# Performance work log

Hardware: AMD Instinct MI355X
Metric: run time of the kernel (lower is better)

The kernel has to match this reference:

```python
import jax, jax.numpy as jnp
import numpy as np
from jax import lax

DN = ('NCHW', 'OIHW', 'NCHW')

def conv(x, w, b, stride, pad):
    y = lax.conv_general_dilated(x, w, (stride, stride), [(pad, pad), (pad, pad)], dimension_numbers=DN)
    return y + b[None, :, None, None]

def setup_inputs() -> dict:
    key = jax.random.key(0)
    ks = jax.random.split(key, 16)
    s = 0.05
    inp = {
        'condition': jax.random.normal(ks[0], (16, 1, 256, 256), jnp.float32),
        'w1': jax.random.normal(ks[1], (64, 1, 4, 4), jnp.float32) * s,
        'b1': jnp.zeros((64,), jnp.float32),
        'w2': jax.random.normal(ks[2], (128, 64, 4, 4), jnp.float32) * s,
        'b2': jnp.zeros((128,), jnp.float32),
        'w3': jax.random.normal(ks[3], (128, 128, 3, 3), jnp.float32) * s,
        'b3': jnp.zeros((128,), jnp.float32),
        'r1w1': jax.random.normal(ks[4], (32, 128, 3, 3), jnp.float32) * s,
        'r1b1': jnp.zeros((32,), jnp.float32),
        'r1w2': jax.random.normal(ks[5], (128, 32, 1, 1), jnp.float32) * s,
        'r1b2': jnp.zeros((128,), jnp.float32),
        'r2w1': jax.random.normal(ks[6], (32, 128, 3, 3), jnp.float32) * s,
        'r2b1': jnp.zeros((32,), jnp.float32),
        'r2w2': jax.random.normal(ks[7], (128, 32, 1, 1), jnp.float32) * s,
        'r2b2': jnp.zeros((128,), jnp.float32),
        'wpre': jax.random.normal(ks[8], (4, 128, 1, 1), jnp.float32) * s,
        'bpre': jnp.zeros((4,), jnp.float32),
        'codebook': jax.random.normal(ks[9], (2048, 4), jnp.float32),
    }
    return inp

def reference(condition, w1, b1, w2, b2, w3, b3, r1w1, r1b1, r1w2, r1b2,
              r2w1, r2b1, r2w2, r2b2, wpre, bpre, codebook):
    # --- conv encoder (VQ-VAE standard) ---
    h = jax.nn.relu(conv(condition, w1, b1, 2, 1))   # [B,64,128,128]
    h = jax.nn.relu(conv(h, w2, b2, 2, 1))           # [B,128,64,64]
    h = conv(h, w3, b3, 1, 1)                        # [B,128,64,64]
    # residual stack: 2 blocks of relu->3x3->relu->1x1, residual add
    for wa, ba, wb, bb in ((r1w1, r1b1, r1w2, r1b2), (r2w1, r2b1, r2w2, r2b2)):
        t = conv(jax.nn.relu(h), wa, ba, 1, 1)
        t = conv(jax.nn.relu(t), wb, bb, 1, 0)
        h = h + t
    h = jax.nn.relu(h)
    z = conv(h, wpre, bpre, 1, 0)                    # [B,4,64,64]
    # --- cosine-distance vector quantization ---
    B, D, H, W = z.shape
    zf = jnp.transpose(z, (0, 2, 3, 1)).reshape(-1, D)          # [BHW, D]
    zn = zf / (jnp.linalg.norm(zf, axis=-1, keepdims=True) + 1e-12)
    en = codebook / (jnp.linalg.norm(codebook, axis=-1, keepdims=True) + 1e-12)
    sim = jnp.einsum('nd,kd->nk', zn, en)                       # cosine similarity
    idx = jnp.argmax(sim, axis=-1)                              # nearest code
    q = codebook[idx].reshape(B, H, W, D)
    c = jnp.transpose(q, (0, 3, 1, 2))                          # [B,4,64,64]
    return c
```

## Files before the change

kernel.cpp:

```cpp
#include <hip/hip_runtime.h>
#include <math.h>


typedef short v8s __attribute__((ext_vector_type(8)));
typedef float v4f __attribute__((ext_vector_type(4)));

#define B_OFF 4194304
#define A_OFF 12582912
#define W2_S 0
#define W3_S 393216
#define WR1_S 835584
#define WR2_S 946176
#define WP1_S 1056768
#define WP2_S 1069056

__device__ inline void limb3(float v, unsigned short& h, unsigned short& m,
                             unsigned short& l) {
    unsigned ub = __float_as_uint(v);
    unsigned hb = ub & 0xffff0000u;
    float r1 = v - __uint_as_float(hb);
    unsigned mb = __float_as_uint(r1) & 0xffff0000u;
    float r2 = r1 - __uint_as_float(mb);
    unsigned lb = __float_as_uint(r2) & 0xffff0000u;
    h = (unsigned short)(hb >> 16);
    m = (unsigned short)(mb >> 16);
    l = (unsigned short)(lb >> 16);
}

struct CfgConv2 {
    static constexpr int NC = 8, NT = 4, OC = 128, ICG = 64, IN_H = 128, IN_W = 128;
    static constexpr bool RELU_IN = false, RELU_OUT = true;
    __device__ static void tap(int c, int t, int& ry, int& rx) {
        int py = (c >> 2) & 1, px = (c >> 1) & 1;
        ry = (t >> 1) - py; rx = (t & 1) - px;
    }
    __device__ static void inaddr(int c, int oy, int r, int X,
                                  int& Yg, int& Xg, int& ic0) {
        int py = (c >> 2) & 1, px = (c >> 1) & 1;
        Yg = 2 * (oy + r - 1) + py; Xg = 2 * X + px; ic0 = (c & 1) * 32;
    }
    __device__ static int widx(int c, int t, int oc, int ic) {
        int py = (c >> 2) & 1, px = (c >> 1) & 1, half = c & 1;
        int dy = 2 * (t >> 1) + (1 - py), dx = 2 * (t & 1) + (1 - px);
        return ((oc * 64 + half * 32 + ic) * 4 + dy) * 4 + dx;
    }
};
struct CfgConv3 {
    static constexpr int NC = 4, NT = 9, OC = 128, ICG = 128, IN_H = 64, IN_W = 64;
    static constexpr bool RELU_IN = false, RELU_OUT = false;
    __device__ static void tap(int c, int t, int& ry, int& rx) {
        ry = t / 3 - 1; rx = t % 3 - 1;
    }
    __device__ static void inaddr(int c, int oy, int r, int X,
                                  int& Yg, int& Xg, int& ic0) {
        Yg = oy + r - 1; Xg = X; ic0 = c * 32;
    }
    __device__ static int widx(int c, int t, int oc, int ic) {
        return ((oc * 128 + c * 32 + ic) * 3 + t / 3) * 3 + t % 3;
    }
};
struct CfgRes {
    static constexpr int NC = 4, NT = 9, OC = 32, ICG = 128, IN_H = 64, IN_W = 64;
    __device__ static int widx(int c, int t, int oc, int ic) {
        return ((oc * 128 + c * 32 + ic) * 3 + t / 3) * 3 + t % 3;
    }
};
struct Cfg1x1 {
    static constexpr int NC = 1, NT = 1, OC = 128;
    __device__ static int widx(int c, int t, int oc, int ic) {
        return oc * 32 + ic;
    }
};

template <typename C>
__device__ inline void repack_one(const float* __restrict__ w,
                                  short* __restrict__ dst, int idx) {
    int s  = idx & 31;
    int oc = (idx >> 5) % C::OC;
    int ct = idx / (32 * C::OC);
    int c = ct / C::NT, t = ct % C::NT;
    float val = w[C::widx(c, t, oc, s)];
    unsigned short h, m, l;
    limb3(val, h, m, l);
    constexpr int NTILE = C::OC / 16;
    int nt = oc >> 4, o = oc & 15, q = s >> 3, j = s & 7;
    int fr = ((q * 16 + o) << 3) + j;
    dst[(((ct * 3 + 0) * NTILE + nt) << 9) + fr] = (short)h;
    dst[(((ct * 3 + 1) * NTILE + nt) << 9) + fr] = (short)m;
    dst[(((ct * 3 + 2) * NTILE + nt) << 9) + fr] = (short)l;
}

__global__ __launch_bounds__(256) void repack_all_k(
    const float* __restrict__ w2, const float* __restrict__ w3,
    const float* __restrict__ r1, const float* __restrict__ r2,
    const float* __restrict__ p1, const float* __restrict__ p2,
    short* __restrict__ base)
{
    int idx = blockIdx.x * 256 + threadIdx.x;
    if (idx < 131072) { repack_one<CfgConv2>(w2, base + W2_S, idx); return; }
    idx -= 131072;
    if (idx < 147456) { repack_one<CfgConv3>(w3, base + W3_S, idx); return; }
    idx -= 147456;
    if (idx < 36864)  { repack_one<CfgRes>(r1, base + WR1_S, idx); return; }
    idx -= 36864;
    if (idx < 36864)  { repack_one<CfgRes>(r2, base + WR2_S, idx); return; }
    idx -= 36864;
    if (idx < 4096)   { repack_one<Cfg1x1>(p1, base + WP1_S, idx); return; }
    idx -= 4096;
    if (idx < 4096)   { repack_one<Cfg1x1>(p2, base + WP2_S, idx); }
}

template <typename C>
__global__ __launch_bounds__(256, 3) void mfma_conv(
    const float* __restrict__ in, const short* __restrict__ repw,
    const float* __restrict__ bias, float* __restrict__ out, int n0)
{
    constexpr int APLANE = 3 * 66 * 32;
    constexpr int NTILE  = C::OC / 16;
    __shared__ __align__(16) short lA[3 * APLANE];

    int tid = threadIdx.x;
    int lane = tid & 63, wv = tid >> 6;
    int n_img = blockIdx.x >> 6, oy = blockIdx.x & 63;

    for (int idx = tid; idx < 3 * 3 * 2 * 16; idx += 256) {
        int plane = idx / 96;
        int rem = idx % 96;
        int rr = rem / 32;
        int hc = (rem / 16) & 1;
        int d = idx & 15;
        ((unsigned*)lA)[plane * 3168 + (rr * 66 + hc * 65) * 16 + d] = 0;
    }

    v4f acc[4][2] = {};
    int nbase = wv * 2;
    int Xq = tid & 15, icp = tid >> 4, quad = lane >> 4;

    float pv[24];
    auto issue_loads = [&](int c) {
#pragma unroll
        for (int it = 0; it < 12; it++) {
            int r = it >> 2, xg = it & 3;
            int X = xg * 16 + Xq;
            int Yg, Xg, ic0;
            C::inaddr(c, oy, r, X, Yg, Xg, ic0);
            float v0 = 0.f, v1 = 0.f;
            if (Yg >= 0 && Yg < C::IN_H) {
                int g = ((n_img * C::ICG + ic0 + 2 * icp) * C::IN_H + Yg) * C::IN_W + Xg;
                v0 = in[g];
                v1 = in[g + C::IN_H * C::IN_W];
            }
            pv[2 * it] = v0; pv[2 * it + 1] = v1;
        }
    };
    auto load_bf = [&](int c, int t, v8s (&dst)[2][3]) {
#pragma unroll
        for (int nt = 0; nt < 2; nt++)
#pragma unroll
            for (int L = 0; L < 3; L++)
                dst[nt][L] = *(const v8s*)(repw +
                    ((((c * C::NT + t) * 3 + L) * NTILE + (nbase + nt)) << 9) +
                    (lane << 3));
    };

    issue_loads(0);

    for (int c = 0; c < C::NC; c++) {
        __syncthreads();
#pragma unroll
        for (int it = 0; it < 12; it++) {
            int r = it >> 2, xg = it & 3;
            int X = xg * 16 + Xq;
            float v0 = pv[2 * it], v1 = pv[2 * it + 1];
            if constexpr (C::RELU_IN) { v0 = fmaxf(v0, 0.f); v1 = fmaxf(v1, 0.f); }
            unsigned short h0, m0, l0, h1, m1, l1;
            limb3(v0, h0, m0, l0);
            limb3(v1, h1, m1, l1);
            int cell = r * 66 + X + 1;
            int f = (cell + (cell >> 2)) & 3;
            int phys = (icp & 3) + 4 * (((icp >> 2) + f) & 3);
            unsigned* pa = (unsigned*)lA + cell * 16 + phys;
            pa[0]        = (unsigned)h0 | ((unsigned)h1 << 16);
            pa[3168]     = (unsigned)m0 | ((unsigned)m1 << 16);
            pa[2 * 3168] = (unsigned)l0 | ((unsigned)l1 << 16);
        }
        __syncthreads();
        if (c + 1 < C::NC) issue_loads(c + 1);

        v8s bf[2][2][3];
        load_bf(c, 0, bf[0]);
#pragma unroll
        for (int t = 0; t < C::NT; t++) {
            constexpr int NTT = C::NT;
            if (t + 1 < NTT) load_bf(c, t + 1, bf[(t + 1) & 1]);
            int ry, rx;
            C::tap(c, t, ry, rx);
#pragma unroll
            for (int mt = 0; mt < 4; mt++) {
                int x = mt * 16 + (lane & 15);
                int cell = (ry + 1) * 66 + (x + rx + 1);
                int f = (cell + (cell >> 2)) & 3;
                int aa = cell * 32 + (((quad + f) & 3) << 3);
                v8s ah = *(const v8s*)&lA[aa];
                v8s am = *(const v8s*)&lA[APLANE + aa];
                v8s al = *(const v8s*)&lA[2 * APLANE + aa];
#pragma unroll
                for (int nt = 0; nt < 2; nt++) {
                    v4f a0 = acc[mt][nt];
                    a0 = __builtin_amdgcn_mfma_f32_16x16x32_bf16(ah, bf[t & 1][nt][0], a0, 0, 0, 0);
                    a0 = __builtin_amdgcn_mfma_f32_16x16x32_bf16(ah, bf[t & 1][nt][1], a0, 0, 0, 0);
                    a0 = __builtin_amdgcn_mfma_f32_16x16x32_bf16(am, bf[t & 1][nt][0], a0, 0, 0, 0);
                    a0 = __builtin_amdgcn_mfma_f32_16x16x32_bf16(am, bf[t & 1][nt][1], a0, 0, 0, 0);
                    a0 = __builtin_amdgcn_mfma_f32_16x16x32_bf16(ah, bf[t & 1][nt][2], a0, 0, 0, 0);
                    a0 = __builtin_amdgcn_mfma_f32_16x16x32_bf16(al, bf[t & 1][nt][0], a0, 0, 0, 0);
                    acc[mt][nt] = a0;
                }
            }
        }
    }
#pragma unroll
    for (int mt = 0; mt < 4; mt++) {
        int x0 = mt * 16 + quad * 4;
#pragma unroll
        for (int nt = 0; nt < 2; nt++) {
            int oc = (nbase + nt) * 16 + (lane & 15);
            float bv = bias[oc];
            float v0 = acc[mt][nt][0] + bv;
            float v1 = acc[mt][nt][1] + bv;
            float v2 = acc[mt][nt][2] + bv;
            float v3 = acc[mt][nt][3] + bv;
            if constexpr (C::RELU_OUT) {
                v0 = fmaxf(v0, 0.f); v1 = fmaxf(v1, 0.f);
                v2 = fmaxf(v2, 0.f); v3 = fmaxf(v3, 0.f);
            }
            float4 o = make_float4(v0, v1, v2, v3);
            *(float4*)&out[(((n0 + n_img) * C::OC + oc) * 64 + oy) * 64 + x0] = o;
        }
    }
}

__global__ __launch_bounds__(256, 4) void mfma_res(
    const float* __restrict__ in, const short* __restrict__ repw,
    const float* __restrict__ b1, const short* __restrict__ repp,
    const float* __restrict__ b2, float* __restrict__ out)
{
    constexpr int APLANE = 3 * 66 * 32;
    __shared__ __align__(16) short lA[3 * APLANE];

    int tid = threadIdx.x;
    int lane = tid & 63, wv = tid >> 6;
    int n_img = blockIdx.x >> 6, oy = blockIdx.x & 63;

    for (int idx = tid; idx < 3 * 3 * 2 * 16; idx += 256) {
        int plane = idx / 96;
        int rem = idx % 96;
        int rr = rem / 32;
        int hc = (rem / 16) & 1;
        int d = idx & 15;
        ((unsigned*)lA)[plane * 3168 + (rr * 66 + hc * 65) * 16 + d] = 0;
    }

    v4f acc[2] = {};
    int Xq = tid & 15, icp = tid >> 4, quad = lane >> 4;

    float pv[24];
    auto issue_loads = [&](int c) {
#pragma unroll
        for (int it = 0; it < 12; it++) {
            int r = it >> 2, xg = it & 3;
            int X = xg * 16 + Xq;
            int Yg = oy + r - 1;
            float v0 = 0.f, v1 = 0.f;
            if (Yg >= 0 && Yg < 64) {
                int g = ((n_img * 128 + c * 32 + 2 * icp) * 64 + Yg) * 64 + X;
                v0 = in[g];
                v1 = in[g + 4096];
            }
            pv[2 * it] = v0; pv[2 * it + 1] = v1;
        }
    };

    issue_loads(0);

    for (int c = 0; c < 4; c++) {
        __syncthreads();
#pragma unroll
        for (int it = 0; it < 12; it++) {
            int r = it >> 2, xg = it & 3;
            int X = xg * 16 + Xq;
            float v0 = fmaxf(pv[2 * it], 0.f);
            float v1 = fmaxf(pv[2 * it + 1], 0.f);
            unsigned short h0, m0, l0, h1, m1, l1;
            limb3(v0, h0, m0, l0);
            limb3(v1, h1, m1, l1);
            int cell = r * 66 + X + 1;
            int f = (cell + (cell >> 2)) & 3;
            int phys = (icp & 3) + 4 * (((icp >> 2) + f) & 3);
            unsigned* pa = (unsigned*)lA + cell * 16 + phys;
            pa[0]        = (unsigned)h0 | ((unsigned)h1 << 16);
            pa[3168]     = (unsigned)m0 | ((unsigned)m1 << 16);
            pa[2 * 3168] = (unsigned)l0 | ((unsigned)l1 << 16);
        }
        __syncthreads();
        if (c + 1 < 4) issue_loads(c + 1);

        v8s bf[2][2][3];
        auto load_bf = [&](int t, v8s (&dst)[2][3]) {
#pragma unroll
            for (int nt = 0; nt < 2; nt++)
#pragma unroll
                for (int L = 0; L < 3; L++)
                    dst[nt][L] = *(const v8s*)(repw +
                        ((((c * 9 + t) * 3 + L) * 2 + nt) << 9) + (lane << 3));
        };
        load_bf(0, bf[0]);
#pragma unroll
        for (int t = 0; t < 9; t++) {
            if (t + 1 < 9) load_bf(t + 1, bf[(t + 1) & 1]);
            int ry = t / 3 - 1, rx = t % 3 - 1;
            int x = wv * 16 + (lane & 15);
            int cell = (ry + 1) * 66 + (x + rx + 1);
            int f = (cell + (cell >> 2)) & 3;
            int aa = cell * 32 + (((quad + f) & 3) << 3);
            v8s ah = *(const v8s*)&lA[aa];
            v8s am = *(const v8s*)&lA[APLANE + aa];
            v8s al = *(const v8s*)&lA[2 * APLANE + aa];
#pragma unroll
            for (int nt = 0; nt < 2; nt++) {
                v4f a0 = acc[nt];
                a0 = __builtin_amdgcn_mfma_f32_16x16x32_bf16(ah, bf[t & 1][nt][0], a0, 0, 0, 0);
                a0 = __builtin_amdgcn_mfma_f32_16x16x32_bf16(ah, bf[t & 1][nt][1], a0, 0, 0, 0);
                a0 = __builtin_amdgcn_mfma_f32_16x16x32_bf16(am, bf[t & 1][nt][0], a0, 0, 0, 0);
                a0 = __builtin_amdgcn_mfma_f32_16x16x32_bf16(am, bf[t & 1][nt][1], a0, 0, 0, 0);
                a0 = __builtin_amdgcn_mfma_f32_16x16x32_bf16(ah, bf[t & 1][nt][2], a0, 0, 0, 0);
                a0 = __builtin_amdgcn_mfma_f32_16x16x32_bf16(al, bf[t & 1][nt][0], a0, 0, 0, 0);
                acc[nt] = a0;
            }
        }
    }

    __syncthreads();
#pragma unroll
    for (int nt = 0; nt < 2; nt++) {
        int ic = nt * 16 + (lane & 15);
        int icp2 = ic >> 1, hilo = ic & 1;
        float bv = b1[ic];
#pragma unroll
        for (int r = 0; r < 4; r++) {
            int x = wv * 16 + quad * 4 + r;
            float v = fmaxf(acc[nt][r] + bv, 0.f);
            unsigned short h, m, l;
            limb3(v, h, m, l);
            int f = (x + (x >> 2)) & 3;
            int phys = (icp2 & 3) + 4 * (((icp2 >> 2) + f) & 3);
            int sa = x * 32 + phys * 2 + hilo;
            lA[sa] = (short)h;
            lA[2048 + sa] = (short)m;
            lA[4096 + sa] = (short)l;
        }
    }
    __syncthreads();

    v4f a2[8] = {};
    {
        int x = wv * 16 + (lane & 15);
        int f = (x + (x >> 2)) & 3;
        int aa = x * 32 + (((quad + f) & 3) << 3);
        v8s ah = *(const v8s*)&lA[aa];
        v8s am = *(const v8s*)&lA[2048 + aa];
        v8s al = *(const v8s*)&lA[4096 + aa];
#pragma unroll
        for (int nt = 0; nt < 8; nt++) {
            v8s bh = *(const v8s*)(repp + ((0 * 8 + nt) << 9) + (lane << 3));
            v8s bm = *(const v8s*)(repp + ((1 * 8 + nt) << 9) + (lane << 3));
            v8s bl = *(const v8s*)(repp + ((2 * 8 + nt) << 9) + (lane << 3));
            v4f a0 = a2[nt];
            a0 = __builtin_amdgcn_mfma_f32_16x16x32_bf16(ah, bh, a0, 0, 0, 0);
            a0 = __builtin_amdgcn_mfma_f32_16x16x32_bf16(ah, bm, a0, 0, 0, 0);
            a0 = __builtin_amdgcn_mfma_f32_16x16x32_bf16(am, bh, a0, 0, 0, 0);
            a0 = __builtin_amdgcn_mfma_f32_16x16x32_bf16(am, bm, a0, 0, 0, 0);
            a0 = __builtin_amdgcn_mfma_f32_16x16x32_bf16(ah, bl, a0, 0, 0, 0);
            a0 = __builtin_amdgcn_mfma_f32_16x16x32_bf16(al, bh, a0, 0, 0, 0);
            a2[nt] = a0;
        }
    }
#pragma unroll
    for (int nt = 0; nt < 8; nt++) {
        int oc = nt * 16 + (lane & 15);
        int x0 = wv * 16 + quad * 4;
        int off = ((n_img * 128 + oc) * 64 + oy) * 64 + x0;
        float4 hv = *(const float4*)&in[off];
        float bv = b2[oc];
        float4 o = make_float4(hv.x + a2[nt][0] + bv, hv.y + a2[nt][1] + bv,
                               hv.z + a2[nt][2] + bv, hv.w + a2[nt][3] + bv);
        *(float4*)&out[off] = o;
    }
}

__global__ __launch_bounds__(256) void conv1_k(
    const float* __restrict__ x, const float* __restrict__ w,
    const float* __restrict__ b, float* __restrict__ out)
{
    int tid = blockIdx.x * 256 + threadIdx.x;
    int n   = tid >> 14;
    int rem = tid & 16383;
    int oy  = rem >> 7;
    int ox  = rem & 127;
    int iy0 = oy * 2 - 1, ix0 = ox * 2 - 1;
    const float* xb = x + n * 65536;
    float v[16];
#pragma unroll
    for (int ky = 0; ky < 4; ky++) {
#pragma unroll
        for (int kx = 0; kx < 4; kx++) {
            int iy = iy0 + ky, ix = ix0 + kx;
            bool ok = (iy >= 0) & (iy < 256) & (ix >= 0) & (ix < 256);
            v[ky * 4 + kx] = ok ? xb[iy * 256 + ix] : 0.f;
        }
    }
    int obase = (n * 64) * 16384 + (oy << 7) + ox;
    for (int oc = 0; oc < 64; oc++) {
        float acc = b[oc];
        const float* wp = w + oc * 16;
#pragma unroll
        for (int k = 0; k < 16; k++) acc = fmaf(v[k], wp[k], acc);
        out[obase + oc * 16384] = fmaxf(acc, 0.f);
    }
}

__global__ __launch_bounds__(256) void prevq_k(
    const float* __restrict__ h, const float* __restrict__ wpre,
    const float* __restrict__ bpre, const float* __restrict__ cb,
    float* __restrict__ out)
{
    __shared__ float4 en[2048];
    for (int i = threadIdx.x; i < 2048; i += 256) {
        float c0 = cb[i * 4 + 0], c1 = cb[i * 4 + 1];
        float c2 = cb[i * 4 + 2], c3 = cb[i * 4 + 3];
        float nrm = sqrtf(c0 * c0 + c1 * c1 + c2 * c2 + c3 * c3) + 1e-12f;
        en[i] = make_float4(c0 / nrm, c1 / nrm, c2 / nrm, c3 / nrm);
    }
    __syncthreads();

    int tid = blockIdx.x * 256 + threadIdx.x;
    int n   = tid >> 12;
    int pos = tid & 4095;
    const float* hb = h + n * 128 * 4096 + pos;
    float z0 = bpre[0], z1 = bpre[1], z2 = bpre[2], z3 = bpre[3];
    for (int ic = 0; ic < 128; ic++) {
        float v = fmaxf(hb[ic * 4096], 0.f);
        z0 = fmaf(v, wpre[ic],       z0);
        z1 = fmaf(v, wpre[128 + ic], z1);
        z2 = fmaf(v, wpre[256 + ic], z2);
        z3 = fmaf(v, wpre[384 + ic], z3);
    }
    float best = -1e30f;
    int   bidx = 0;
    for (int k = 0; k < 2048; k++) {
        float4 e = en[k];
        float s = z0 * e.x + z1 * e.y + z2 * e.z + z3 * e.w;
        if (s > best) { best = s; bidx = k; }
    }
    const float* q = cb + bidx * 4;
    out[(n * 4 + 0) * 4096 + pos] = q[0];
    out[(n * 4 + 1) * 4096 + pos] = q[1];
    out[(n * 4 + 2) * 4096 + pos] = q[2];
    out[(n * 4 + 3) * 4096 + pos] = q[3];
}

extern "C" void kernel_launch(void* const* d_in, const int* in_sizes, int n_in,
                              void* d_out, int out_size, void* d_ws, size_t ws_size,
                              hipStream_t stream)
{
    const float* x    = (const float*)d_in[0];
    const float* w1   = (const float*)d_in[1];
    const float* b1   = (const float*)d_in[2];
    const float* w2   = (const float*)d_in[3];
    const float* b2   = (const float*)d_in[4];
    const float* w3   = (const float*)d_in[5];
    const float* b3   = (const float*)d_in[6];
    const float* r1w1 = (const float*)d_in[7];
    const float* r1b1 = (const float*)d_in[8];
    const float* r1w2 = (const float*)d_in[9];
    const float* r1b2 = (const float*)d_in[10];
    const float* r2w1 = (const float*)d_in[11];
    const float* r2b1 = (const float*)d_in[12];
    const float* r2w2 = (const float*)d_in[13];
    const float* r2b2 = (const float*)d_in[14];
    const float* wpre = (const float*)d_in[15];
    const float* bpre = (const float*)d_in[16];
    const float* cb   = (const float*)d_in[17];
    float* out = (float*)d_out;

    float* ws   = (float*)d_ws;
    short* wsS  = (short*)d_ws;
    float* B = ws + B_OFF;
    float* A = ws + A_OFF;

    repack_all_k<<<1408, 256, 0, stream>>>(w2, w3, r1w1, r2w1, r1w2, r2w2, wsS);

    conv1_k<<<512, 256, 0, stream>>>(x,               w1, b1, A);
    mfma_conv<CfgConv2><<<512, 256, 0, stream>>>(A, wsS + W2_S, b2, B, 0);
    conv1_k<<<512, 256, 0, stream>>>(x + 8 * 65536,   w1, b1, A);
    mfma_conv<CfgConv2><<<512, 256, 0, stream>>>(A, wsS + W2_S, b2, B, 8);

    mfma_conv<CfgConv3><<<1024, 256, 0, stream>>>(B, wsS + W3_S, b3, A, 0);

    mfma_res<<<1024, 256, 0, stream>>>(A, wsS + WR1_S, r1b1, wsS + WP1_S, r1b2, B);
    mfma_res<<<1024, 256, 0, stream>>>(B, wsS + WR2_S, r2b1, wsS + WP2_S, r2b2, A);

    prevq_k<<<256, 256, 0, stream>>>(A, wpre, bpre, cb, out);
}
```

Measured before the change: 485.0 us.

## Double-buffer LDS input tiles and interleave staging with MFMA taps

The conv kernel now keeps two LDS buffers and two register prefetch sets. It stages the next chunk's bf16 limbs into the alternate buffer in slices interleaved between the MFMA tap iterations, and prefetches two chunks ahead, so one barrier per chunk replaces two. The goal is to hide the global-load and conversion latency behind matrix math. In exchange LDS use doubles, register pressure rises, and launch bounds drop from 3 to 2 blocks per CU, which lowers occupancy.

```diff
diff --git a/kernel.cpp b/kernel.cpp
--- a/kernel.cpp
+++ b/kernel.cpp
@@ -111,33 +111,26 @@
 }
 
 template <typename C>
-__global__ __launch_bounds__(256, 3) void mfma_conv(
+__global__ __launch_bounds__(256, 2) void mfma_conv(
     const float* __restrict__ in, const short* __restrict__ repw,
     const float* __restrict__ bias, float* __restrict__ out, int n0)
 {
     constexpr int APLANE = 3 * 66 * 32;
+    constexpr int BUFS   = 3 * APLANE;
     constexpr int NTILE  = C::OC / 16;
-    __shared__ __align__(16) short lA[3 * APLANE];
+    __shared__ __align__(16) short lA[2 * BUFS];
 
     int tid = threadIdx.x;
     int lane = tid & 63, wv = tid >> 6;
     int n_img = blockIdx.x >> 6, oy = blockIdx.x & 63;
 
-    for (int idx = tid; idx < 3 * 3 * 2 * 16; idx += 256) {
-        int plane = idx / 96;
-        int rem = idx % 96;
-        int rr = rem / 32;
-        int hc = (rem / 16) & 1;
-        int d = idx & 15;
-        ((unsigned*)lA)[plane * 3168 + (rr * 66 + hc * 65) * 16 + d] = 0;
-    }
-
-    v4f acc[4][2] = {};
     int nbase = wv * 2;
     int Xq = tid & 15, icp = tid >> 4, quad = lane >> 4;
 
-    float pv[24];
-    auto issue_loads = [&](int c) {
+    v4f acc[4][2] = {};
+    float pvA[24], pvB[24];
+
+    auto issue_loads = [&](int c, float* pv) {
 #pragma unroll
         for (int it = 0; it < 12; it++) {
             int r = it >> 2, xg = it & 3;
@@ -153,6 +146,22 @@
             pv[2 * it] = v0; pv[2 * it + 1] = v1;
         }
     };
+    auto stage_it = [&](int it, short* dst, const float* pv) {
+        int r = it >> 2, xg = it & 3;
+        int X = xg * 16 + Xq;
+        float v0 = pv[2 * it], v1 = pv[2 * it + 1];
+        if constexpr (C::RELU_IN) { v0 = fmaxf(v0, 0.f); v1 = fmaxf(v1, 0.f); }
+        unsigned short h0, m0, l0, h1, m1, l1;
+        limb3(v0, h0, m0, l0);
+        limb3(v1, h1, m1, l1);
+        int cell = r * 66 + X + 1;
+        int f = (cell + (cell >> 2)) & 3;
+        int phys = (icp & 3) + 4 * (((icp >> 2) + f) & 3);
+        unsigned* pa = (unsigned*)dst + cell * 16 + phys;
+        pa[0]        = (unsigned)h0 | ((unsigned)h1 << 16);
+        pa[3168]     = (unsigned)m0 | ((unsigned)m1 << 16);
+        pa[2 * 3168] = (unsigned)l0 | ((unsigned)l1 << 16);
+    };
     auto load_bf = [&](int c, int t, v8s (&dst)[2][3]) {
 #pragma unroll
         for (int nt = 0; nt < 2; nt++)
@@ -163,30 +172,10 @@
                     (lane << 3));
     };
 
-    issue_loads(0);
-
-    for (int c = 0; c < C::NC; c++) {
-        __syncthreads();
-#pragma unroll
-        for (int it = 0; it < 12; it++) {
-            int r = it >> 2, xg = it & 3;
-            int X = xg * 16 + Xq;
-            float v0 = pv[2 * it], v1 = pv[2 * it + 1];
-            if constexpr (C::RELU_IN) { v0 = fmaxf(v0, 0.f); v1 = fmaxf(v1, 0.f); }
-            unsigned short h0, m0, l0, h1, m1, l1;
-            limb3(v0, h0, m0, l0);
-            limb3(v1, h1, m1, l1);
-            int cell = r * 66 + X + 1;
-            int f = (cell + (cell >> 2)) & 3;
-            int phys = (icp & 3) + 4 * (((icp >> 2) + f) & 3);
-            unsigned* pa = (unsigned*)lA + cell * 16 + phys;
-            pa[0]        = (unsigned)h0 | ((unsigned)h1 << 16);
-            pa[3168]     = (unsigned)m0 | ((unsigned)m1 << 16);
-            pa[2 * 3168] = (unsigned)l0 | ((unsigned)l1 << 16);
-        }
-        __syncthreads();
-        if (c + 1 < C::NC) issue_loads(c + 1);
-
+    auto run_chunk = [&](int c, const short* cur, short* nxt,
+                         const float* pvr, float* pvw) {
+        if (c + 2 < C::NC) issue_loads(c + 2, pvw);
+        const bool do_stage = (c + 1 < C::NC);
         v8s bf[2][2][3];
         load_bf(c, 0, bf[0]);
 #pragma unroll
@@ -201,9 +190,9 @@
                 int cell = (ry + 1) * 66 + (x + rx + 1);
                 int f = (cell + (cell >> 2)) & 3;
                 int aa = cell * 32 + (((quad + f) & 3) << 3);
-                v8s ah = *(const v8s*)&lA[aa];
-                v8s am = *(const v8s*)&lA[APLANE + aa];
-                v8s al = *(const v8s*)&lA[2 * APLANE + aa];
+                v8s ah = *(const v8s*)&cur[aa];
+                v8s am = *(const v8s*)&cur[APLANE + aa];
+                v8s al = *(const v8s*)&cur[2 * APLANE + aa];
 #pragma unroll
                 for (int nt = 0; nt < 2; nt++) {
                     v4f a0 = acc[mt][nt];
@@ -216,8 +205,38 @@
                     acc[mt][nt] = a0;
                 }
             }
-        }
-    }
+            if (do_stage) {
+#pragma unroll
+                for (int it = (t * 12) / NTT; it < ((t + 1) * 12) / NTT; it++)
+                    stage_it(it, nxt, pvr);
+            }
+        }
+    };
+
+    issue_loads(0, pvA);
+    issue_loads(1, pvB);
+    for (int idx = tid; idx < 2 * 3 * 3 * 2 * 16; idx += 256) {
+        int buf = idx / 288;
+        int rem = idx % 288;
+        int plane = rem / 96;
+        int rem2 = rem % 96;
+        int rr = rem2 / 32;
+        int hc = (rem2 / 16) & 1;
+        int d = idx & 15;
+        ((unsigned*)lA)[buf * (BUFS / 2) + plane * 3168 + (rr * 66 + hc * 65) * 16 + d] = 0;
+    }
+#pragma unroll
+    for (int it = 0; it < 12; it++) stage_it(it, lA, pvA);
+    __syncthreads();
+
+    for (int c = 0; c < C::NC; c++) {
+        const short* cur = lA + (c & 1) * BUFS;
+        short* nxt = lA + ((c & 1) ^ 1) * BUFS;
+        if ((c & 1) == 0) run_chunk(c, cur, nxt, pvB, pvA);
+        else              run_chunk(c, cur, nxt, pvA, pvB);
+        if (c + 1 < C::NC) __syncthreads();
+    }
+
 #pragma unroll
     for (int mt = 0; mt < 4; mt++) {
         int x0 = mt * 16 + quad * 4;
```

After: 552.8 us. +14.0%, slower.

## Remap mfma_conv waves to 2x2 M/N tiling and split weight prefetch

Applied to the files above, without the earlier changes.

Changes the warp tiling in the MFMA conv kernel: each of 4 waves now computes 2 M-tiles by 4 N-tiles instead of 4 M-tiles by 2 N-tiles. Per tap this halves the LDS A-fragment reads per wave and doubles the global weight fragment loads. Weight loading is split into two halves interleaved with the MFMA groups, which replaces the full double buffer and keeps register pressure down. The risk is more global/L2 traffic for weights, traded against less LDS bandwidth use.

```diff
diff --git a/kernel.cpp b/kernel.cpp
--- a/kernel.cpp
+++ b/kernel.cpp
@@ -117,6 +117,7 @@
 {
     constexpr int APLANE = 3 * 66 * 32;
     constexpr int NTILE  = C::OC / 16;
+    constexpr int NTT    = C::NT;
     __shared__ __align__(16) short lA[3 * APLANE];
 
     int tid = threadIdx.x;
@@ -132,8 +133,9 @@
         ((unsigned*)lA)[plane * 3168 + (rr * 66 + hc * 65) * 16 + d] = 0;
     }
 
-    v4f acc[4][2] = {};
-    int nbase = wv * 2;
+    int mr = wv >> 1, nc = wv & 1;
+    int nbase = nc * 4;
+    v4f acc[2][4] = {};
     int Xq = tid & 15, icp = tid >> 4, quad = lane >> 4;
 
     float pv[24];
@@ -153,13 +155,13 @@
             pv[2 * it] = v0; pv[2 * it + 1] = v1;
         }
     };
-    auto load_bf = [&](int c, int t, v8s (&dst)[2][3]) {
-#pragma unroll
-        for (int nt = 0; nt < 2; nt++)
+    auto load_half = [&](int c, int t, int hp, v8s (&dst)[2][3]) {
+#pragma unroll
+        for (int j = 0; j < 2; j++)
 #pragma unroll
             for (int L = 0; L < 3; L++)
-                dst[nt][L] = *(const v8s*)(repw +
-                    ((((c * C::NT + t) * 3 + L) * NTILE + (nbase + nt)) << 9) +
+                dst[j][L] = *(const v8s*)(repw +
+                    ((((c * NTT + t) * 3 + L) * NTILE + (nbase + hp * 2 + j)) << 9) +
                     (lane << 3));
     };
 
@@ -187,48 +189,64 @@
         __syncthreads();
         if (c + 1 < C::NC) issue_loads(c + 1);
 
-        v8s bf[2][2][3];
-        load_bf(c, 0, bf[0]);
-#pragma unroll
-        for (int t = 0; t < C::NT; t++) {
-            constexpr int NTT = C::NT;
-            if (t + 1 < NTT) load_bf(c, t + 1, bf[(t + 1) & 1]);
+        v8s bf0[2][3], bf1[2][3];
+        load_half(c, 0, 0, bf0);
+#pragma unroll
+        for (int t = 0; t < NTT; t++) {
             int ry, rx;
             C::tap(c, t, ry, rx);
-#pragma unroll
-            for (int mt = 0; mt < 4; mt++) {
-                int x = mt * 16 + (lane & 15);
+            v8s ah[2], am[2], al[2];
+#pragma unroll
+            for (int mti = 0; mti < 2; mti++) {
+                int x = (mr * 2 + mti) * 16 + (lane & 15);
                 int cell = (ry + 1) * 66 + (x + rx + 1);
                 int f = (cell + (cell >> 2)) & 3;
                 int aa = cell * 32 + (((quad + f) & 3) << 3);
-                v8s ah = *(const v8s*)&lA[aa];
-                v8s am = *(const v8s*)&lA[APLANE + aa];
-                v8s al = *(const v8s*)&lA[2 * APLANE + aa];
-#pragma unroll
-                for (int nt = 0; nt < 2; nt++) {
-                    v4f a0 = acc[mt][nt];
-                    a0 = __builtin_amdgcn_mfma_f32_16x16x32_bf16(ah, bf[t & 1][nt][0], a0, 0, 0, 0);
-                    a0 = __builtin_amdgcn_mfma_f32_16x16x32_bf16(ah, bf[t & 1][nt][1], a0, 0, 0, 0);
-                    a0 = __builtin_amdgcn_mfma_f32_16x16x32_bf16(am, bf[t & 1][nt][0], a0, 0, 0, 0);
-                    a0 = __builtin_amdgcn_mfma_f32_16x16x32_bf16(am, bf[t & 1][nt][1], a0, 0, 0, 0);
-                    a0 = __builtin_amdgcn_mfma_f32_16x16x32_bf16(ah, bf[t & 1][nt][2], a0, 0, 0, 0);
-                    a0 = __builtin_amdgcn_mfma_f32_16x16x32_bf16(al, bf[t & 1][nt][0], a0, 0, 0, 0);
-                    acc[mt][nt] = a0;
+                ah[mti] = *(const v8s*)&lA[aa];
+                am[mti] = *(const v8s*)&lA[APLANE + aa];
+                al[mti] = *(const v8s*)&lA[2 * APLANE + aa];
+            }
+            load_half(c, t, 1, bf1);
+#pragma unroll
+            for (int mti = 0; mti < 2; mti++)
+#pragma unroll
+                for (int j = 0; j < 2; j++) {
+                    v4f a0 = acc[mti][j];
+                    a0 = __builtin_amdgcn_mfma_f32_16x16x32_bf16(ah[mti], bf0[j][0], a0, 0, 0, 0);
+                    a0 = __builtin_amdgcn_mfma_f32_16x16x32_bf16(ah[mti], bf0[j][1], a0, 0, 0, 0);
+                    a0 = __builtin_amdgcn_mfma_f32_16x16x32_bf16(am[mti], bf0[j][0], a0, 0, 0, 0);
+                    a0 = __builtin_amdgcn_mfma_f32_16x16x32_bf16(am[mti], bf0[j][1], a0, 0, 0, 0);
+                    a0 = __builtin_amdgcn_mfma_f32_16x16x32_bf16(ah[mti], bf0[j][2], a0, 0, 0, 0);
+                    a0 = __builtin_amdgcn_mfma_f32_16x16x32_bf16(al[mti], bf0[j][0], a0, 0, 0, 0);
+                    acc[mti][j] = a0;
                 }
-            }
-        }
-    }
-#pragma unroll
-    for (int mt = 0; mt < 4; mt++) {
-        int x0 = mt * 16 + quad * 4;
-#pragma unroll
-        for (int nt = 0; nt < 2; nt++) {
+            if (t + 1 < NTT) load_half(c, t + 1, 0, bf0);
+#pragma unroll
+            for (int mti = 0; mti < 2; mti++)
+#pragma unroll
+                for (int j = 0; j < 2; j++) {
+                    v4f a0 = acc[mti][2 + j];
+                    a0 = __builtin_amdgcn_mfma_f32_16x16x32_bf16(ah[mti], bf1[j][0], a0, 0, 0, 0);
+                    a0 = __builtin_amdgcn_mfma_f32_16x16x32_bf16(ah[mti], bf1[j][1], a0, 0, 0, 0);
+                    a0 = __builtin_amdgcn_mfma_f32_16x16x32_bf16(am[mti], bf1[j][0], a0, 0, 0, 0);
+                    a0 = __builtin_amdgcn_mfma_f32_16x16x32_bf16(am[mti], bf1[j][1], a0, 0, 0, 0);
+                    a0 = __builtin_amdgcn_mfma_f32_16x16x32_bf16(ah[mti], bf1[j][2], a0, 0, 0, 0);
+                    a0 = __builtin_amdgcn_mfma_f32_16x16x32_bf16(al[mti], bf1[j][0], a0, 0, 0, 0);
+                    acc[mti][2 + j] = a0;
+                }
+        }
+    }
+#pragma unroll
+    for (int mti = 0; mti < 2; mti++) {
+        int x0 = (mr * 2 + mti) * 16 + quad * 4;
+#pragma unroll
+        for (int nt = 0; nt < 4; nt++) {
             int oc = (nbase + nt) * 16 + (lane & 15);
             float bv = bias[oc];
-            float v0 = acc[mt][nt][0] + bv;
-            float v1 = acc[mt][nt][1] + bv;
-            float v2 = acc[mt][nt][2] + bv;
-            float v3 = acc[mt][nt][3] + bv;
+            float v0 = acc[mti][nt][0] + bv;
+            float v1 = acc[mti][nt][1] + bv;
+            float v2 = acc[mti][nt][2] + bv;
+            float v3 = acc[mti][nt][3] + bv;
             if constexpr (C::RELU_OUT) {
                 v0 = fmaxf(v0, 0.f); v1 = fmaxf(v1, 0.f);
                 v2 = fmaxf(v2, 0.f); v3 = fmaxf(v3, 0.f);
```

After: 499.0 us. +2.9%, slower.

## Compute two output rows per block in conv3 and residual kernels

Applied to the files above, without the earlier changes.

Conv3 and the residual-block kernels now produce two output rows per workgroup. A four-row input halo is staged in LDS, so each pair of rows shares its overlapping halo rows, and each B-fragment weight load is reused across both rows. This halves the grid and the per-row weight and halo traffic. In exchange it uses more registers and LDS, lowers the occupancy target from 3 or 4 to 2, and leaves fewer blocks for the GPU's many compute units.

```diff
diff --git a/kernel.cpp b/kernel.cpp
--- a/kernel.cpp
+++ b/kernel.cpp
@@ -29,15 +29,16 @@
 
 struct CfgConv2 {
     static constexpr int NC = 8, NT = 4, OC = 128, ICG = 64, IN_H = 128, IN_W = 128;
+    static constexpr int OYB = 1;
     static constexpr bool RELU_IN = false, RELU_OUT = true;
     __device__ static void tap(int c, int t, int& ry, int& rx) {
         int py = (c >> 2) & 1, px = (c >> 1) & 1;
         ry = (t >> 1) - py; rx = (t & 1) - px;
     }
-    __device__ static void inaddr(int c, int oy, int r, int X,
+    __device__ static void inaddr(int c, int oy0, int r, int X,
                                   int& Yg, int& Xg, int& ic0) {
         int py = (c >> 2) & 1, px = (c >> 1) & 1;
-        Yg = 2 * (oy + r - 1) + py; Xg = 2 * X + px; ic0 = (c & 1) * 32;
+        Yg = 2 * (oy0 + r - 1) + py; Xg = 2 * X + px; ic0 = (c & 1) * 32;
     }
     __device__ static int widx(int c, int t, int oc, int ic) {
         int py = (c >> 2) & 1, px = (c >> 1) & 1, half = c & 1;
@@ -47,13 +48,14 @@
 };
 struct CfgConv3 {
     static constexpr int NC = 4, NT = 9, OC = 128, ICG = 128, IN_H = 64, IN_W = 64;
+    static constexpr int OYB = 2;
     static constexpr bool RELU_IN = false, RELU_OUT = false;
     __device__ static void tap(int c, int t, int& ry, int& rx) {
         ry = t / 3 - 1; rx = t % 3 - 1;
     }
-    __device__ static void inaddr(int c, int oy, int r, int X,
+    __device__ static void inaddr(int c, int oy0, int r, int X,
                                   int& Yg, int& Xg, int& ic0) {
-        Yg = oy + r - 1; Xg = X; ic0 = c * 32;
+        Yg = oy0 + r - 1; Xg = X; ic0 = c * 32;
     }
     __device__ static int widx(int c, int t, int oc, int ic) {
         return ((oc * 128 + c * 32 + ic) * 3 + t / 3) * 3 + t % 3;
@@ -111,39 +113,46 @@
 }
 
 template <typename C>
-__global__ __launch_bounds__(256, 3) void mfma_conv(
+__global__ __launch_bounds__(256, 2) void mfma_conv(
     const float* __restrict__ in, const short* __restrict__ repw,
     const float* __restrict__ bias, float* __restrict__ out, int n0)
 {
-    constexpr int APLANE = 3 * 66 * 32;
-    constexpr int NTILE  = C::OC / 16;
-    __shared__ __align__(16) short lA[3 * APLANE];
+    constexpr int OYB     = C::OYB;
+    constexpr int WR      = OYB + 2;
+    constexpr int PLANE_D = WR * 66 * 16;
+    constexpr int PLANE_S = 2 * PLANE_D;
+    constexpr int NTILE   = C::OC / 16;
+    constexpr int NTT     = C::NT;
+    constexpr int NIT     = WR * 4;
+    constexpr int ROWS    = 64 / OYB;
+    __shared__ __align__(16) short lA[3 * PLANE_S];
 
     int tid = threadIdx.x;
     int lane = tid & 63, wv = tid >> 6;
-    int n_img = blockIdx.x >> 6, oy = blockIdx.x & 63;
-
-    for (int idx = tid; idx < 3 * 3 * 2 * 16; idx += 256) {
-        int plane = idx / 96;
-        int rem = idx % 96;
+    int n_img = blockIdx.x / ROWS;
+    int oy0 = (blockIdx.x % ROWS) * OYB;
+
+    for (int idx = tid; idx < 3 * WR * 2 * 16; idx += 256) {
+        int plane = idx / (WR * 32);
+        int rem = idx % (WR * 32);
         int rr = rem / 32;
-        int hc = (rem / 16) & 1;
+        int hc = (rem >> 4) & 1;
         int d = idx & 15;
-        ((unsigned*)lA)[plane * 3168 + (rr * 66 + hc * 65) * 16 + d] = 0;
-    }
-
-    v4f acc[4][2] = {};
+        ((unsigned*)lA)[plane * PLANE_D + (rr * 66 + hc * 65) * 16 + d] = 0;
+    }
+
     int nbase = wv * 2;
+    v4f acc[OYB][4][2] = {};
     int Xq = tid & 15, icp = tid >> 4, quad = lane >> 4;
 
-    float pv[24];
+    float pv[2 * NIT];
     auto issue_loads = [&](int c) {
 #pragma unroll
-        for (int it = 0; it < 12; it++) {
+        for (int it = 0; it < NIT; it++) {
             int r = it >> 2, xg = it & 3;
             int X = xg * 16 + Xq;
             int Yg, Xg, ic0;
-            C::inaddr(c, oy, r, X, Yg, Xg, ic0);
+            C::inaddr(c, oy0, r, X, Yg, Xg, ic0);
             float v0 = 0.f, v1 = 0.f;
             if (Yg >= 0 && Yg < C::IN_H) {
                 int g = ((n_img * C::ICG + ic0 + 2 * icp) * C::IN_H + Yg) * C::IN_W + Xg;
@@ -159,7 +168,7 @@
 #pragma unroll
             for (int L = 0; L < 3; L++)
                 dst[nt][L] = *(const v8s*)(repw +
-                    ((((c * C::NT + t) * 3 + L) * NTILE + (nbase + nt)) << 9) +
+                    ((((c * NTT + t) * 3 + L) * NTILE + (nbase + nt)) << 9) +
                     (lane << 3));
     };
 
@@ -168,7 +177,7 @@
     for (int c = 0; c < C::NC; c++) {
         __syncthreads();
 #pragma unroll
-        for (int it = 0; it < 12; it++) {
+        for (int it = 0; it < NIT; it++) {
             int r = it >> 2, xg = it & 3;
             int X = xg * 16 + Xq;
             float v0 = pv[2 * it], v1 = pv[2 * it + 1];
@@ -180,9 +189,9 @@
             int f = (cell + (cell >> 2)) & 3;
             int phys = (icp & 3) + 4 * (((icp >> 2) + f) & 3);
             unsigned* pa = (unsigned*)lA + cell * 16 + phys;
-            pa[0]        = (unsigned)h0 | ((unsigned)h1 << 16);
-            pa[3168]     = (unsigned)m0 | ((unsigned)m1 << 16);
-            pa[2 * 3168] = (unsigned)l0 | ((unsigned)l1 << 16);
+            pa[0]            = (unsigned)h0 | ((unsigned)h1 << 16);
+            pa[PLANE_D]      = (unsigned)m0 | ((unsigned)m1 << 16);
+            pa[2 * PLANE_D]  = (unsigned)l0 | ((unsigned)l1 << 16);
         }
         __syncthreads();
         if (c + 1 < C::NC) issue_loads(c + 1);
@@ -190,86 +199,93 @@
         v8s bf[2][2][3];
         load_bf(c, 0, bf[0]);
 #pragma unroll
-        for (int t = 0; t < C::NT; t++) {
-            constexpr int NTT = C::NT;
+        for (int t = 0; t < NTT; t++) {
             if (t + 1 < NTT) load_bf(c, t + 1, bf[(t + 1) & 1]);
             int ry, rx;
             C::tap(c, t, ry, rx);
 #pragma unroll
-            for (int mt = 0; mt < 4; mt++) {
-                int x = mt * 16 + (lane & 15);
-                int cell = (ry + 1) * 66 + (x + rx + 1);
-                int f = (cell + (cell >> 2)) & 3;
-                int aa = cell * 32 + (((quad + f) & 3) << 3);
-                v8s ah = *(const v8s*)&lA[aa];
-                v8s am = *(const v8s*)&lA[APLANE + aa];
-                v8s al = *(const v8s*)&lA[2 * APLANE + aa];
-#pragma unroll
-                for (int nt = 0; nt < 2; nt++) {
-                    v4f a0 = acc[mt][nt];
-                    a0 = __builtin_amdgcn_mfma_f32_16x16x32_bf16(ah, bf[t & 1][nt][0], a0, 0, 0, 0);
-                    a0 = __builtin_amdgcn_mfma_f32_16x16x32_bf16(ah, bf[t & 1][nt][1], a0, 0, 0, 0);
-                    a0 = __builtin_amdgcn_mfma_f32_16x16x32_bf16(am, bf[t & 1][nt][0], a0, 0, 0, 0);
-                    a0 = __builtin_amdgcn_mfma_f32_16x16x32_bf16(am, bf[t & 1][nt][1], a0, 0, 0, 0);
-                    a0 = __builtin_amdgcn_mfma_f32_16x16x32_bf16(ah, bf[t & 1][nt][2], a0, 0, 0, 0);
-                    a0 = __builtin_amdgcn_mfma_f32_16x16x32_bf16(al, bf[t & 1][nt][0], a0, 0, 0, 0);
-                    acc[mt][nt] = a0;
+            for (int j = 0; j < OYB; j++) {
+#pragma unroll
+                for (int mt = 0; mt < 4; mt++) {
+                    int x = mt * 16 + (lane & 15);
+                    int cell = (j + ry + 1) * 66 + (x + rx + 1);
+                    int f = (cell + (cell >> 2)) & 3;
+                    int aa = cell * 32 + (((quad + f) & 3) << 3);
+                    v8s ah = *(const v8s*)&lA[aa];
+                    v8s am = *(const v8s*)&lA[PLANE_S + aa];
+                    v8s al = *(const v8s*)&lA[2 * PLANE_S + aa];
+#pragma unroll
+                    for (int nt = 0; nt < 2; nt++) {
+                        v4f a0 = acc[j][mt][nt];
+                        a0 = __builtin_amdgcn_mfma_f32_16x16x32_bf16(ah, bf[t & 1][nt][0], a0, 0, 0, 0);
+                        a0 = __builtin_amdgcn_mfma_f32_16x16x32_bf16(ah, bf[t & 1][nt][1], a0, 0, 0, 0);
+                        a0 = __builtin_amdgcn_mfma_f32_16x16x32_bf16(am, bf[t & 1][nt][0], a0, 0, 0, 0);
+                        a0 = __builtin_amdgcn_mfma_f32_16x16x32_bf16(am, bf[t & 1][nt][1], a0, 0, 0, 0);
+                        a0 = __builtin_amdgcn_mfma_f32_16x16x32_bf16(ah, bf[t & 1][nt][2], a0, 0, 0, 0);
+                        a0 = __builtin_amdgcn_mfma_f32_16x16x32_bf16(al, bf[t & 1][nt][0], a0, 0, 0, 0);
+                        acc[j][mt][nt] = a0;
+                    }
                 }
             }
         }
     }
 #pragma unroll
-    for (int mt = 0; mt < 4; mt++) {
-        int x0 = mt * 16 + quad * 4;
-#pragma unroll
-        for (int nt = 0; nt < 2; nt++) {
-            int oc = (nbase + nt) * 16 + (lane & 15);
-            float bv = bias[oc];
-            float v0 = acc[mt][nt][0] + bv;
-            float v1 = acc[mt][nt][1] + bv;
-            float v2 = acc[mt][nt][2] + bv;
-            float v3 = acc[mt][nt][3] + bv;
-            if constexpr (C::RELU_OUT) {
-                v0 = fmaxf(v0, 0.f); v1 = fmaxf(v1, 0.f);
-                v2 = fmaxf(v2, 0.f); v3 = fmaxf(v3, 0.f);
+    for (int j = 0; j < OYB; j++) {
+#pragma unroll
+        for (int mt = 0; mt < 4; mt++) {
+            int x0 = mt * 16 + quad * 4;
+#pragma unroll
+            for (int nt = 0; nt < 2; nt++) {
+                int oc = (nbase + nt) * 16 + (lane & 15);
+                float bv = bias[oc];
+                float v0 = acc[j][mt][nt][0] + bv;
+                float v1 = acc[j][mt][nt][1] + bv;
+                float v2 = acc[j][mt][nt][2] + bv;
+                float v3 = acc[j][mt][nt][3] + bv;
+                if constexpr (C::RELU_OUT) {
+                    v0 = fmaxf(v0, 0.f); v1 = fmaxf(v1, 0.f);
+                    v2 = fmaxf(v2, 0.f); v3 = fmaxf(v3, 0.f);
+                }
+                float4 o = make_float4(v0, v1, v2, v3);
+                *(float4*)&out[(((n0 + n_img) * C::OC + oc) * 64 + (oy0 + j)) * 64 + x0] = o;
             }
-            float4 o = make_float4(v0, v1, v2, v3);
-            *(float4*)&out[(((n0 + n_img) * C::OC + oc) * 64 + oy) * 64 + x0] = o;
-        }
-    }
-}
-
-__global__ __launch_bounds__(256, 4) void mfma_res(
+        }
+    }
+}
+
+__global__ __launch_bounds__(256, 2) void mfma_res(
     const float* __restrict__ in, const short* __restrict__ repw,
     const float* __restrict__ b1, const short* __restrict__ repp,
     const float* __restrict__ b2, float* __restrict__ out)
 {
-    constexpr int APLANE = 3 * 66 * 32;
-    __shared__ __align__(16) short lA[3 * APLANE];
+    constexpr int PLANE_D = 4 * 66 * 16;
+    constexpr int PLANE_S = 2 * PLANE_D;
+    __shared__ __align__(16) short lA[3 * PLANE_S];
 
     int tid = threadIdx.x;
     int lane = tid & 63, wv = tid >> 6;
-    int n_img = blockIdx.x >> 6, oy = blockIdx.x & 63;
-
-    for (int idx = tid; idx < 3 * 3 * 2 * 16; idx += 256) {
-        int plane = idx / 96;
-        int rem = idx % 96;
+    int n_img = blockIdx.x >> 5;
+    int oy0 = (blockIdx.x & 31) << 1;
+
+    for (int idx = tid; idx < 3 * 4 * 2 * 16; idx += 256) {
+        int plane = idx / 128;
+        int rem = idx % 128;
         int rr = rem / 32;
-        int hc = (rem / 16) & 1;
+        int hc = (rem >> 4) & 1;
         int d = idx & 15;
-        ((unsigned*)lA)[plane * 3168 + (rr * 66 + hc * 65) * 16 + d] = 0;
-    }
-
-    v4f acc[2] = {};
+        ((unsigned*)lA)[plane * PLANE_D + (rr * 66 + hc * 65) * 16 + d] = 0;
+    }
+
+    v4f acc[2][2] = {};
     int Xq = tid & 15, icp = tid >> 4, quad = lane >> 4;
 
-    float pv[24];
+    float pv[32];
     auto issue_loads = [&](int c) {
 #pragma unroll
-        for (int it = 0; it < 12; it++) {
+        for (int it = 0; it < 16; it++) {
             int r = it >> 2, xg = it & 3;
             int X = xg * 16 + Xq;
-            int Yg = oy + r - 1;
+            int Yg = oy0 + r - 1;
             float v0 = 0.f, v1 = 0.f;
             if (Yg >= 0 && Yg < 64) {
                 int g = ((n_img * 128 + c * 32 + 2 * icp) * 64 + Yg) * 64 + X;
@@ -285,7 +301,7 @@
     for (int c = 0; c < 4; c++) {
         __syncthreads();
 #pragma unroll
-        for (int it = 0; it < 12; it++) {
+        for (int it = 0; it < 16; it++) {
             int r = it >> 2, xg = it & 3;
             int X = xg * 16 + Xq;
             float v0 = fmaxf(pv[2 * it], 0.f);
@@ -297,9 +313,9 @@
             int f = (cell + (cell >> 2)) & 3;
             int phys = (icp & 3) + 4 * (((icp >> 2) + f) & 3);
             unsigned* pa = (unsigned*)lA + cell * 16 + phys;
-            pa[0]        = (unsigned)h0 | ((unsigned)h1 << 16);
-            pa[3168]     = (unsigned)m0 | ((unsigned)m1 << 16);
-            pa[2 * 3168] = (unsigned)l0 | ((unsigned)l1 << 16);
+            pa[0]           = (unsigned)h0 | ((unsigned)h1 << 16);
+            pa[PLANE_D]     = (unsigned)m0 | ((unsigned)m1 << 16);
+            pa[2 * PLANE_D] = (unsigned)l0 | ((unsigned)l1 << 16);
         }
         __syncthreads();
         if (c + 1 < 4) issue_loads(c + 1);
@@ -318,82 +334,96 @@
         for (int t = 0; t < 9; t++) {
             if (t + 1 < 9) load_bf(t + 1, bf[(t + 1) & 1]);
             int ry = t / 3 - 1, rx = t % 3 - 1;
-            int x = wv * 16 + (lane & 15);
-            int cell = (ry + 1) * 66 + (x + rx + 1);
-            int f = (cell + (cell >> 2)) & 3;
-            int aa = cell * 32 + (((quad + f) & 3) << 3);
-            v8s ah = *(const v8s*)&lA[aa];
-            v8s am = *(const v8s*)&lA[APLANE + aa];
-            v8s al = *(const v8s*)&lA[2 * APLANE + aa];
-#pragma unroll
-            for (int nt = 0; nt < 2; nt++) {
-                v4f a0 = acc[nt];
-                a0 = __builtin_amdgcn_mfma_f32_16x16x32_bf16(ah, bf[t & 1][nt][0], a0, 0, 0, 0);
-                a0 = __builtin_amdgcn_mfma_f32_16x16x32_bf16(ah, bf[t & 1][nt][1], a0, 0, 0, 0);
-                a0 = __builtin_amdgcn_mfma_f32_16x16x32_bf16(am, bf[t & 1][nt][0], a0, 0, 0, 0);
-                a0 = __builtin_amdgcn_mfma_f32_16x16x32_bf16(am, bf[t & 1][nt][1], a0, 0, 0, 0);
-                a0 = __builtin_amdgcn_mfma_f32_16x16x32_bf16(ah, bf[t & 1][nt][2], a0, 0, 0, 0);
-                a0 = __builtin_amdgcn_mfma_f32_16x16x32_bf16(al, bf[t & 1][nt][0], a0, 0, 0, 0);
-                acc[nt] = a0;
+#pragma unroll
+            for (int j = 0; j < 2; j++) {
+                int x = wv * 16 + (lane & 15);
+                int cell = (j + ry + 1) * 66 + (x + rx + 1);
+                int f = (cell + (cell >> 2)) & 3;
+                int aa = cell * 32 + (((quad + f) & 3) << 3);
+                v8s ah = *(const v8s*)&lA[aa];
+                v8s am = *(const v8s*)&lA[PLANE_S + aa];
+                v8s al = *(const v8s*)&lA[2 * PLANE_S + aa];
+#pragma unroll
+                for (int nt = 0; nt < 2; nt++) {
+                    v4f a0 = acc[j][nt];
+                    a0 = __builtin_amdgcn_mfma_f32_16x16x32_bf16(ah, bf[t & 1][nt][0], a0, 0, 0, 0);
+                    a0 = __builtin_amdgcn_mfma_f32_16x16x32_bf16(ah, bf[t & 1][nt][1], a0, 0, 0, 0);
+                    a0 = __builtin_amdgcn_mfma_f32_16x16x32_bf16(am, bf[t & 1][nt][0], a0, 0, 0, 0);
+                    a0 = __builtin_amdgcn_mfma_f32_16x16x32_bf16(am, bf[t & 1][nt][1], a0, 0, 0, 0);
+                    a0 = __builtin_amdgcn_mfma_f32_16x16x32_bf16(ah, bf[t & 1][nt][2], a0, 0, 0, 0);
+                    a0 = __builtin_amdgcn_mfma_f32_16x16x32_bf16(al, bf[t & 1][nt][0], a0, 0, 0, 0);
+                    acc[j][nt] = a0;
+                }
             }
         }
     }
 
     __syncthreads();
 #pragma unroll
-    for (int nt = 0; nt < 2; nt++) {
-        int ic = nt * 16 + (lane & 15);
-        int icp2 = ic >> 1, hilo = ic & 1;
-        float bv = b1[ic];
-#pragma unroll
-        for (int r = 0; r < 4; r++) {
-            int x = wv * 16 + quad * 4 + r;
-            float v = fmaxf(acc[nt][r] + bv, 0.f);
-            unsigned short h, m, l;
-            limb3(v, h, m, l);
-            int f = (x + (x >> 2)) & 3;
-            int phys = (icp2 & 3) + 4 * (((icp2 >> 2) + f) & 3);
-            int sa = x * 32 + phys * 2 + hilo;
-            lA[sa] = (short)h;
-            lA[2048 + sa] = (short)m;
-            lA[4096 + sa] = (short)l;
+    for (int j = 0; j < 2; j++) {
+#pragma unroll
+        for (int nt = 0; nt < 2; nt++) {
+            int ic = nt * 16 + (lane & 15);
+            int icp2 = ic >> 1, hilo = ic & 1;
+            float bv = b1[ic];
+#pragma unroll
+            for (int r = 0; r < 4; r++) {
+                int x = wv * 16 + quad * 4 + r;
+                float v = fmaxf(acc[j][nt][r] + bv, 0.f);
+                unsigned short h, m, l;
+                limb3(v, h, m, l);
+                int f = (x + (x >> 2)) & 3;
+                int phys = (icp2 & 3) + 4 * (((icp2 >> 2) + f) & 3);
+                int sa = x * 32 + phys * 2 + hilo;
+                lA[j * 6144 + sa]        = (short)h;
+                lA[j * 6144 + 2048 + sa] = (short)m;
+                lA[j * 6144 + 4096 + sa] = (short)l;
+            }
         }
     }
     __syncthreads();
 
-    v4f a2[8] = {};
-    {
+    v4f a2[2][8] = {};
+    v8s ah[2], am[2], al[2];
+#pragma unroll
+    for (int j = 0; j < 2; j++) {
         int x = wv * 16 + (lane & 15);
         int f = (x + (x >> 2)) & 3;
         int aa = x * 32 + (((quad + f) & 3) << 3);
-        v8s ah = *(const v8s*)&lA[aa];
-        v8s am = *(const v8s*)&lA[2048 + aa];
-        v8s al = *(const v8s*)&lA[4096 + aa];
+        ah[j] = *(const v8s*)&lA[j * 6144 + aa];
+        am[j] = *(const v8s*)&lA[j * 6144 + 2048 + aa];
+        al[j] = *(const v8s*)&lA[j * 6144 + 4096 + aa];
+    }
+#pragma unroll
+    for (int nt = 0; nt < 8; nt++) {
+        v8s bh = *(const v8s*)(repp + ((0 * 8 + nt) << 9) + (lane << 3));
+        v8s bm = *(const v8s*)(repp + ((1 * 8 + nt) << 9) + (lane << 3));
+        v8s bl = *(const v8s*)(repp + ((2 * 8 + nt) << 9) + (lane << 3));
+#pragma unroll
+        for (int j = 0; j < 2; j++) {
+            v4f a0 = a2[j][nt];
+            a0 = __builtin_amdgcn_mfma_f32_16x16x32_bf16(ah[j], bh, a0, 0, 0, 0);
+            a0 = __builtin_amdgcn_mfma_f32_16x16x32_bf16(ah[j], bm, a0, 0, 0, 0);
+            a0 = __builtin_amdgcn_mfma_f32_16x16x32_bf16(am[j], bh, a0, 0, 0, 0);
+            a0 = __builtin_amdgcn_mfma_f32_16x16x32_bf16(am[j], bm, a0, 0, 0, 0);
+            a0 = __builtin_amdgcn_mfma_f32_16x16x32_bf16(ah[j], bl, a0, 0, 0, 0);
+            a0 = __builtin_amdgcn_mfma_f32_16x16x32_bf16(al[j], bh, a0, 0, 0, 0);
+            a2[j][nt] = a0;
+        }
+    }
+#pragma unroll
+    for (int j = 0; j < 2; j++) {
 #pragma unroll
         for (int nt = 0; nt < 8; nt++) {
-            v8s bh = *(const v8s*)(repp + ((0 * 8 + nt) << 9) + (lane << 3));
-            v8s bm = *(const v8s*)(repp + ((1 * 8 + nt) << 9) + (lane << 3));
-            v8s bl = *(const v8s*)(repp + ((2 * 8 + nt) << 9) + (lane << 3));
-            v4f a0 = a2[nt];
-            a0 = __builtin_amdgcn_mfma_f32_16x16x32_bf16(ah, bh, a0, 0, 0, 0);
-            a0 = __builtin_amdgcn_mfma_f32_16x16x32_bf16(ah, bm, a0, 0, 0, 0);
-            a0 = __builtin_amdgcn_mfma_f32_16x16x32_bf16(am, bh, a0, 0, 0, 0);
-            a0 = __builtin_amdgcn_mfma_f32_16x16x32_bf16(am, bm, a0, 0, 0, 0);
-            a0 = __builtin_amdgcn_mfma_f32_16x16x32_bf16(ah, bl, a0, 0, 0, 0);
-            a0 = __builtin_amdgcn_mfma_f32_16x16x32_bf16(al, bh, a0, 0, 0, 0);
-            a2[nt] = a0;
-        }
-    }
-#pragma unroll
-    for (int nt = 0; nt < 8; nt++) {
-        int oc = nt * 16 + (lane & 15);
-        int x0 = wv * 16 + quad * 4;
-        int off = ((n_img * 128 + oc) * 64 + oy) * 64 + x0;
-        float4 hv = *(const float4*)&in[off];
-        float bv = b2[oc];
-        float4 o = make_float4(hv.x + a2[nt][0] + bv, hv.y + a2[nt][1] + bv,
-                               hv.z + a2[nt][2] + bv, hv.w + a2[nt][3] + bv);
-        *(float4*)&out[off] = o;
+            int oc = nt * 16 + (lane & 15);
+            int x0 = wv * 16 + quad * 4;
+            int off = ((n_img * 128 + oc) * 64 + (oy0 + j)) * 64 + x0;
+            float4 hv = *(const float4*)&in[off];
+            float bv = b2[oc];
+            float4 o = make_float4(hv.x + a2[j][nt][0] + bv, hv.y + a2[j][nt][1] + bv,
+                                   hv.z + a2[j][nt][2] + bv, hv.w + a2[j][nt][3] + bv);
+            *(float4*)&out[off] = o;
+        }
     }
 }
 
@@ -504,10 +534,10 @@
     conv1_k<<<512, 256, 0, stream>>>(x + 8 * 65536,   w1, b1, A);
     mfma_conv<CfgConv2><<<512, 256, 0, stream>>>(A, wsS + W2_S, b2, B, 8);
 
-    mfma_conv<CfgConv3><<<1024, 256, 0, stream>>>(B, wsS + W3_S, b3, A, 0);
-
-    mfma_res<<<1024, 256, 0, stream>>>(A, wsS + WR1_S, r1b1, wsS + WP1_S, r1b2, B);
-    mfma_res<<<1024, 256, 0, stream>>>(B, wsS + WR2_S, r2b1, wsS + WP2_S, r2b2, A);
+    mfma_conv<CfgConv3><<<512, 256, 0, stream>>>(B, wsS + W3_S, b3, A, 0);
+
+    mfma_res<<<512, 256, 0, stream>>>(A, wsS + WR1_S, r1b1, wsS + WP1_S, r1b2, B);
+    mfma_res<<<512, 256, 0, stream>>>(B, wsS + WR2_S, r2b1, wsS + WP2_S, r2b2, A);
 
     prevq_k<<<256, 256, 0, stream>>>(A, wpre, bpre, cb, out);
 }
```

New measurement: 539.3 us. 11.2% more time.
